# Kernel optimization log

Hardware: AMD Instinct MI355X
Metric: run time of the kernel (lower is better)

The kernel has to match this reference:

```python
import jax, jax.numpy as jnp
import numpy as np

NEG_SLOPE = 0.01  # torch nn.LeakyReLU default


def setup_inputs() -> dict:
    key = jax.random.key(0)
    k1, k2, k3, k4, k5 = jax.random.split(key, 5)
    B, C, N, O = 32, 512, 1024, 512
    x = jax.random.normal(k1, (B, C, N), dtype=jnp.float32)
    wq = jax.random.normal(k2, (C,), dtype=jnp.float32) * (1.0 / np.sqrt(C))
    wk = jax.random.normal(k3, (C,), dtype=jnp.float32) * (1.0 / np.sqrt(C))
    wm = jax.random.normal(k4, (O, C), dtype=jnp.float32) * (1.0 / np.sqrt(C))
    bm = jax.random.normal(k5, (O,), dtype=jnp.float32) * 0.01
    return {"x": x, "wq": wq, "wk": wk, "wm": wm, "bm": bm}


def reference(x, wq, wk, wm, bm):
    # x: [B, C, N]
    q = jnp.einsum('c,bcn->bn', wq, x)            # [B, N] (Conv1d C->1, k=1, no bias)
    k = jnp.einsum('c,bcn->bn', wk, x)            # [B, N]
    scores = q[:, None, :] + k[:, :, None]        # [B, N, N] additive broadcast
    scores = jnp.where(scores > 0, scores, NEG_SLOPE * scores)  # LeakyReLU
    att = jax.nn.softmax(scores, axis=-1)         # softmax over last dim
    agg = jnp.einsum('bcn,bmn->bcm', x, att)      # weighted aggregation [B, C, N]
    out = jnp.einsum('oc,bcm->bom', wm, agg) + bm[None, :, None]  # Conv1d k=1
    return jax.nn.relu(out)
```

## Files before the change

### kernel.cpp

```cpp
#include <hip/hip_runtime.h>


constexpr int B = 32, C = 512, N = 1024, O = 512;
constexpr float L2E = 1.4426950408889634f;

typedef _Float16 half8 __attribute__((ext_vector_type(8)));
typedef _Float16 half4v __attribute__((ext_vector_type(4)));
typedef _Float16 half2v __attribute__((ext_vector_type(2)));
typedef float f32x4 __attribute__((ext_vector_type(4)));
typedef float f32x16 __attribute__((ext_vector_type(16)));

#if __has_builtin(__builtin_amdgcn_exp2f)
#define EXP2(x) __builtin_amdgcn_exp2f(x)
#else
#define EXP2(x) exp2f(x)
#endif

__device__ __forceinline__ half8 cvt8(float4 a, float4 b) {
  half8 h;
  h[0] = (_Float16)a.x; h[1] = (_Float16)a.y; h[2] = (_Float16)a.z; h[3] = (_Float16)a.w;
  h[4] = (_Float16)b.x; h[5] = (_Float16)b.y; h[6] = (_Float16)b.z; h[7] = (_Float16)b.w;
  return h;
}

__device__ __forceinline__ unsigned fenc(float x) {
  unsigned u = __float_as_uint(x);
  return (u & 0x80000000u) ? ~u : (u ^ 0x80000000u);
}
__device__ __forceinline__ float fdec(unsigned e) {
  unsigned u = (e & 0x80000000u) ? (e ^ 0x80000000u) : ~e;
  return __uint_as_float(u);
}

__global__ __launch_bounds__(256) void wmh_kernel(const float* __restrict__ wm,
                                                  _Float16* __restrict__ wmh,
                                                  unsigned* __restrict__ qmax_u) {
  int i = (blockIdx.x * 256 + threadIdx.x) * 8;
  float4 a = *(const float4*)(wm + i);
  float4 b = *(const float4*)(wm + i + 4);
  *(half8*)(wmh + i) = cvt8(a, b);
  if (blockIdx.x == 0 && threadIdx.x < 64) qmax_u[threadIdx.x] = 0u;
}

__global__ __launch_bounds__(256) void gemm_y_kernel(const float* __restrict__ x,
    const _Float16* __restrict__ wmh, const float* __restrict__ wq,
    const float* __restrict__ wk, float* __restrict__ q, float* __restrict__ k,
    unsigned* __restrict__ qmax_u, _Float16* __restrict__ Yt) {
  __shared__ half2v Xs[2][16 * 130];
  __shared__ float mred[4];
  int b  = blockIdx.y;
  int n0 = blockIdx.x * 128;
  int o0 = blockIdx.z * 128;
  int t = threadIdx.x;
  int w = t >> 6, l = t & 63;
  int nw = w >> 1, ow = w & 1;
  int lm = l & 15, q8 = (l >> 4) * 8, q4 = (l >> 4) * 4;

  int cp = t >> 4, ng = t & 15;
  bool doqk = (blockIdx.z == 0);
  float aq[8] = {}, ak[8] = {};

  const _Float16* wb[4];
#pragma unroll
  for (int j = 0; j < 4; ++j)
    wb[j] = wmh + (size_t)(o0 + ow * 64 + j * 16 + lm) * C + q8;
  const float* xbase = x + ((size_t)b * C + 2 * cp) * N + n0 + ng * 8;

  float4 a0 = *(const float4*)(xbase);
  float4 a1 = *(const float4*)(xbase + 4);
  float4 b0 = *(const float4*)(xbase + N);
  float4 b1 = *(const float4*)(xbase + N + 4);
  half8 bf[4];
#pragma unroll
  for (int j = 0; j < 4; ++j) bf[j] = *(const half8*)(wb[j]);

  if (doqk) {
    float2 wq2 = *(const float2*)&wq[2 * cp];
    float2 wk2 = *(const float2*)&wk[2 * cp];
    aq[0] = fmaf(wq2.x, a0.x, fmaf(wq2.y, b0.x, aq[0]));
    aq[1] = fmaf(wq2.x, a0.y, fmaf(wq2.y, b0.y, aq[1]));
    aq[2] = fmaf(wq2.x, a0.z, fmaf(wq2.y, b0.z, aq[2]));
    aq[3] = fmaf(wq2.x, a0.w, fmaf(wq2.y, b0.w, aq[3]));
    aq[4] = fmaf(wq2.x, a1.x, fmaf(wq2.y, b1.x, aq[4]));
    aq[5] = fmaf(wq2.x, a1.y, fmaf(wq2.y, b1.y, aq[5]));
    aq[6] = fmaf(wq2.x, a1.z, fmaf(wq2.y, b1.z, aq[6]));
    aq[7] = fmaf(wq2.x, a1.w, fmaf(wq2.y, b1.w, aq[7]));
    ak[0] = fmaf(wk2.x, a0.x, fmaf(wk2.y, b0.x, ak[0]));
    ak[1] = fmaf(wk2.x, a0.y, fmaf(wk2.y, b0.y, ak[1]));
    ak[2] = fmaf(wk2.x, a0.z, fmaf(wk2.y, b0.z, ak[2]));
    ak[3] = fmaf(wk2.x, a0.w, fmaf(wk2.y, b0.w, ak[3]));
    ak[4] = fmaf(wk2.x, a1.x, fmaf(wk2.y, b1.x, ak[4]));
    ak[5] = fmaf(wk2.x, a1.y, fmaf(wk2.y, b1.y, ak[5]));
    ak[6] = fmaf(wk2.x, a1.z, fmaf(wk2.y, b1.z, ak[6]));
    ak[7] = fmaf(wk2.x, a1.w, fmaf(wk2.y, b1.w, ak[7]));
  }
  {
    half2v* xp = &Xs[0][cp * 130 + ng * 8];
    xp[0] = half2v{(_Float16)a0.x, (_Float16)b0.x};
    xp[1] = half2v{(_Float16)a0.y, (_Float16)b0.y};
    xp[2] = half2v{(_Float16)a0.z, (_Float16)b0.z};
    xp[3] = half2v{(_Float16)a0.w, (_Float16)b0.w};
    xp[4] = half2v{(_Float16)a1.x, (_Float16)b1.x};
    xp[5] = half2v{(_Float16)a1.y, (_Float16)b1.y};
    xp[6] = half2v{(_Float16)a1.z, (_Float16)b1.z};
    xp[7] = half2v{(_Float16)a1.w, (_Float16)b1.w};
  }
  __syncthreads();

  f32x4 acc[4][4] = {};
  for (int it = 0; it < 16; ++it) {
    int p = it & 1;
    float4 na0, na1, nb0, nb1;
    half8 nbf[4];
    if (it < 15) {
      int c1 = (it + 1) * 32;
      const float* xr = xbase + (size_t)c1 * N;
      na0 = *(const float4*)(xr);
      na1 = *(const float4*)(xr + 4);
      nb0 = *(const float4*)(xr + N);
      nb1 = *(const float4*)(xr + N + 4);
#pragma unroll
      for (int j = 0; j < 4; ++j) nbf[j] = *(const half8*)(wb[j] + c1);
    }
    half8 af[4];
#pragma unroll
    for (int i = 0; i < 4; ++i) {
      int nrow = nw * 64 + i * 16 + lm;
#pragma unroll
      for (int jp = 0; jp < 4; ++jp) {
        half2v pr = Xs[p][(q4 + jp) * 130 + nrow];
        af[i][2 * jp]     = pr[0];
        af[i][2 * jp + 1] = pr[1];
      }
    }
#pragma unroll
    for (int i = 0; i < 4; ++i)
#pragma unroll
      for (int j = 0; j < 4; ++j)
        acc[i][j] = __builtin_amdgcn_mfma_f32_16x16x32_f16(af[i], bf[j], acc[i][j], 0, 0, 0);

    if (it < 15) {
      int c1 = (it + 1) * 32;
      if (doqk) {
        float2 wq2 = *(const float2*)&wq[c1 + 2 * cp];
        float2 wk2 = *(const float2*)&wk[c1 + 2 * cp];
        aq[0] = fmaf(wq2.x, na0.x, fmaf(wq2.y, nb0.x, aq[0]));
        aq[1] = fmaf(wq2.x, na0.y, fmaf(wq2.y, nb0.y, aq[1]));
        aq[2] = fmaf(wq2.x, na0.z, fmaf(wq2.y, nb0.z, aq[2]));
        aq[3] = fmaf(wq2.x, na0.w, fmaf(wq2.y, nb0.w, aq[3]));
        aq[4] = fmaf(wq2.x, na1.x, fmaf(wq2.y, nb1.x, aq[4]));
        aq[5] = fmaf(wq2.x, na1.y, fmaf(wq2.y, nb1.y, aq[5]));
        aq[6] = fmaf(wq2.x, na1.z, fmaf(wq2.y, nb1.z, aq[6]));
        aq[7] = fmaf(wq2.x, na1.w, fmaf(wq2.y, nb1.w, aq[7]));
        ak[0] = fmaf(wk2.x, na0.x, fmaf(wk2.y, nb0.x, ak[0]));
        ak[1] = fmaf(wk2.x, na0.y, fmaf(wk2.y, nb0.y, ak[1]));
        ak[2] = fmaf(wk2.x, na0.z, fmaf(wk2.y, nb0.z, ak[2]));
        ak[3] = fmaf(wk2.x, na0.w, fmaf(wk2.y, nb0.w, ak[3]));
        ak[4] = fmaf(wk2.x, na1.x, fmaf(wk2.y, nb1.x, ak[4]));
        ak[5] = fmaf(wk2.x, na1.y, fmaf(wk2.y, nb1.y, ak[5]));
        ak[6] = fmaf(wk2.x, na1.z, fmaf(wk2.y, nb1.z, ak[6]));
        ak[7] = fmaf(wk2.x, na1.w, fmaf(wk2.y, nb1.w, ak[7]));
      }
      half2v* xp = &Xs[p ^ 1][cp * 130 + ng * 8];
      xp[0] = half2v{(_Float16)na0.x, (_Float16)nb0.x};
      xp[1] = half2v{(_Float16)na0.y, (_Float16)nb0.y};
      xp[2] = half2v{(_Float16)na0.z, (_Float16)nb0.z};
      xp[3] = half2v{(_Float16)na0.w, (_Float16)nb0.w};
      xp[4] = half2v{(_Float16)na1.x, (_Float16)nb1.x};
      xp[5] = half2v{(_Float16)na1.y, (_Float16)nb1.y};
      xp[6] = half2v{(_Float16)na1.z, (_Float16)nb1.z};
      xp[7] = half2v{(_Float16)na1.w, (_Float16)nb1.w};
#pragma unroll
      for (int j = 0; j < 4; ++j) bf[j] = nbf[j];
    }
    __syncthreads();
  }

#pragma unroll
  for (int i = 0; i < 4; ++i) {
    int n_b = n0 + nw * 64 + i * 16 + (l >> 4) * 4;
#pragma unroll
    for (int j = 0; j < 4; ++j) {
      int o_c = o0 + ow * 64 + j * 16 + lm;
      half4v h;
      h[0] = (_Float16)acc[i][j][0];
      h[1] = (_Float16)acc[i][j][1];
      h[2] = (_Float16)acc[i][j][2];
      h[3] = (_Float16)acc[i][j][3];
      *(half4v*)&Yt[((size_t)b * O + o_c) * N + n_b] = h;
    }
  }

  if (doqk) {
    float* red = (float*)Xs;
    float qv_final = -1e30f;
    __syncthreads();
#pragma unroll
    for (int j = 0; j < 8; ++j) red[cp * 130 + ng * 8 + j] = aq[j];
    __syncthreads();
    if (t < 128) {
      float s = 0.f;
#pragma unroll
      for (int p = 0; p < 16; ++p) s += red[p * 130 + t];
      qv_final = L2E * s;
      q[b * N + n0 + t] = qv_final;
    }
    __syncthreads();
#pragma unroll
    for (int j = 0; j < 8; ++j) red[cp * 130 + ng * 8 + j] = ak[j];
    __syncthreads();
    if (t < 128) {
      float s = 0.f;
#pragma unroll
      for (int p = 0; p < 16; ++p) s += red[p * 130 + t];
      k[b * N + n0 + t] = L2E * s;
    }
    float m = qv_final;
#pragma unroll
    for (int off = 32; off > 0; off >>= 1) m = fmaxf(m, __shfl_down(m, off, 64));
    if ((t & 63) == 0) mred[t >> 6] = m;
    __syncthreads();
    if (t == 0) {
      float bmax = fmaxf(fmaxf(mred[0], mred[1]), fmaxf(mred[2], mred[3]));
      atomicMax(&qmax_u[b], fenc(bmax));
    }
  }
}

__global__ __launch_bounds__(512) void gemm_out_kernel(const _Float16* __restrict__ Yt,
    const float* __restrict__ q, const float* __restrict__ k,
    const unsigned* __restrict__ qmax_u, const float* __restrict__ bm,
    float* __restrict__ out) {
  __shared__ __align__(16) float qs[N];
  __shared__ __align__(16) _Float16 Ys[2][256 * 40];
  __shared__ float izs[256];
  int b  = blockIdx.y;
  int o0 = blockIdx.x * 256;
  int m0 = blockIdx.z * 256;
  int t = threadIdx.x;
  int w = t >> 6, l = t & 63;
  int ml = l & 31, g2 = l >> 5;

  *(float2*)&qs[t * 2] = *(const float2*)&q[b * N + t * 2];

  float qmv = fdec(qmax_u[b]);
  float km = k[b * N + m0 + w * 32 + ml];
  float s0 = qmv + km;
  float M  = fmaxf(s0, 0.01f * s0);
  float kc2 = km - M;
  float kc3 = fmaf(0.01f, km, -M);

  half8 ones;
#pragma unroll
  for (int jj = 0; jj < 8; ++jj) ones[jj] = (_Float16)1.0f;
  f32x16 acc_z = {};
  int yr = t >> 1, yp = t & 1;
  const _Float16* ysrc = Yt + ((size_t)b * O + o0 + yr) * N + yp * 16;

  {
    half8 z0 = *(const half8*)(ysrc);
    half8 z1 = *(const half8*)(ysrc + 8);
    *(half8*)&Ys[0][yr * 40 + yp * 16]     = z0;
    *(half8*)&Ys[0][yr * 40 + yp * 16 + 8] = z1;
  }
  __syncthreads();

  f32x16 acc[8] = {};
  for (int it = 0; it < N / 32; ++it) {
    int p = it & 1;
    int n0k = it * 32;
    half8 z0, z1;
    if (it < N / 32 - 1) {
      z0 = *(const half8*)(ysrc + n0k + 32);
      z1 = *(const half8*)(ysrc + n0k + 40);
    }
#pragma unroll
    for (int kh = 0; kh < 2; ++kh) {
      float4 qa = *(const float4*)&qs[n0k + kh * 16 + g2 * 8];
      float4 qb = *(const float4*)&qs[n0k + kh * 16 + g2 * 8 + 4];
      float qv[8] = {qa.x, qa.y, qa.z, qa.w, qb.x, qb.y, qb.z, qb.w};
      half8 af;
#pragma unroll
      for (int jj = 0; jj < 8; ++jj) {
        float arg = fmaxf(qv[jj] + kc2, fmaf(0.01f, qv[jj], kc3));
        af[jj] = (_Float16)EXP2(arg);
      }
      acc_z = __builtin_amdgcn_mfma_f32_32x32x16_f16(af, ones, acc_z, 0, 0, 0);
#pragma unroll
      for (int s = 0; s < 8; ++s) {
        half8 bf = *(const half8*)&Ys[p][(s * 32 + ml) * 40 + kh * 16 + g2 * 8];
        acc[s] = __builtin_amdgcn_mfma_f32_32x32x16_f16(af, bf, acc[s], 0, 0, 0);
      }
    }
    if (it < N / 32 - 1) {
      *(half8*)&Ys[p ^ 1][yr * 40 + yp * 16]     = z0;
      *(half8*)&Ys[p ^ 1][yr * 40 + yp * 16 + 8] = z1;
    }
    __syncthreads();
  }

  if (ml == 0) {
#pragma unroll
    for (int rq = 0; rq < 4; ++rq)
#pragma unroll
      for (int r = 0; r < 4; ++r)
        izs[w * 32 + r + 8 * rq + 4 * g2] = 1.0f / acc_z[rq * 4 + r];
  }
  __syncthreads();

  float4 izv[4];
#pragma unroll
  for (int rq = 0; rq < 4; ++rq)
    izv[rq] = *(const float4*)&izs[w * 32 + 8 * rq + 4 * g2];

#pragma unroll
  for (int s = 0; s < 8; ++s) {
    int o_c = o0 + s * 32 + ml;
    float bias = bm[o_c];
#pragma unroll
    for (int rq = 0; rq < 4; ++rq) {
      int m_b = m0 + w * 32 + 8 * rq + 4 * g2;
      float4 r;
      r.x = fmaxf(fmaf(acc[s][rq * 4 + 0], izv[rq].x, bias), 0.f);
      r.y = fmaxf(fmaf(acc[s][rq * 4 + 1], izv[rq].y, bias), 0.f);
      r.z = fmaxf(fmaf(acc[s][rq * 4 + 2], izv[rq].z, bias), 0.f);
      r.w = fmaxf(fmaf(acc[s][rq * 4 + 3], izv[rq].w, bias), 0.f);
      *(float4*)&out[((size_t)b * O + o_c) * N + m_b] = r;
    }
  }
}

extern "C" void kernel_launch(void* const* d_in, const int* in_sizes, int n_in,
                              void* d_out, int out_size, void* d_ws, size_t ws_size,
                              hipStream_t stream) {
  const float* x  = (const float*)d_in[0];
  const float* wq = (const float*)d_in[1];
  const float* wk = (const float*)d_in[2];
  const float* wm = (const float*)d_in[3];
  const float* bm = (const float*)d_in[4];
  float* out = (float*)d_out;

  float* q    = (float*)d_ws;
  float* k    = q + B * N;
  unsigned* qmax_u = (unsigned*)(k + B * N);
  _Float16* wmh = (_Float16*)(qmax_u + 64);
  _Float16* Yt  = wmh + (size_t)O * C;

  wmh_kernel<<<dim3(O * C / (256 * 8)), 256, 0, stream>>>(wm, wmh, qmax_u);
  gemm_y_kernel<<<dim3(N / 128, B, O / 128), 256, 0, stream>>>(x, wmh, wq, wk, q, k, qmax_u, Yt);
  gemm_out_kernel<<<dim3(O / 256, B, N / 256), 512, 0, stream>>>(Yt, q, k, qmax_u, bm, out);
}
```

Measured before the change: 205.7 us.

## Split x fp16 transpose into prep kernel and load GEMM tiles via global_load_lds

A new prep kernel converts x to fp16 once, transposed to [B,N,C], and computes q, k and the per-batch q max there, so that work leaves the GEMM. The Y GEMM then streams A tiles directly into LDS with global_load_lds and uses contiguous half8 LDS reads instead of per-element half2 gathers. It also remaps block indices so that tiles sharing data land on the same XCD. The cost is an extra kernel launch and a full fp16 copy of x written to and read back from global memory, using the output buffer as scratch. The original GEMM re-read and re-converted x for each of its four O tiles.

Result: slower. 214.8 us (+4.4%).

```diff
diff --git a/kernel.cpp b/kernel.cpp
--- a/kernel.cpp
+++ b/kernel.cpp
@@ -30,6 +30,12 @@
 __device__ __forceinline__ float fdec(unsigned e) {
   unsigned u = (e & 0x80000000u) ? (e ^ 0x80000000u) : ~e;
   return __uint_as_float(u);
+}
+
+__device__ __forceinline__ void gload16(const _Float16* g, _Float16* l) {
+  __builtin_amdgcn_global_load_lds(
+      (const __attribute__((address_space(1))) unsigned int*)(g),
+      (__attribute__((address_space(3))) unsigned int*)(l), 16, 0, 0);
 }
 
 __global__ __launch_bounds__(256) void wmh_kernel(const float* __restrict__ wm,
@@ -42,41 +48,31 @@
   if (blockIdx.x == 0 && threadIdx.x < 64) qmax_u[threadIdx.x] = 0u;
 }
 
-__global__ __launch_bounds__(256) void gemm_y_kernel(const float* __restrict__ x,
-    const _Float16* __restrict__ wmh, const float* __restrict__ wq,
-    const float* __restrict__ wk, float* __restrict__ q, float* __restrict__ k,
-    unsigned* __restrict__ qmax_u, _Float16* __restrict__ Yt) {
-  __shared__ half2v Xs[2][16 * 130];
-  __shared__ float mred[4];
+__global__ __launch_bounds__(256) void prep_kernel(const float* __restrict__ x,
+    const float* __restrict__ wq, const float* __restrict__ wk,
+    float* __restrict__ q, float* __restrict__ k, unsigned* __restrict__ qmax_u,
+    _Float16* __restrict__ xhT) {
+  __shared__ half2v Ts[32 * 67];
   int b  = blockIdx.y;
-  int n0 = blockIdx.x * 128;
-  int o0 = blockIdx.z * 128;
+  int n0 = blockIdx.x * 64;
   int t = threadIdx.x;
-  int w = t >> 6, l = t & 63;
-  int nw = w >> 1, ow = w & 1;
-  int lm = l & 15, q8 = (l >> 4) * 8, q4 = (l >> 4) * 4;
-
-  int cp = t >> 4, ng = t & 15;
-  bool doqk = (blockIdx.z == 0);
+  int cp = t >> 3;
+  int ng = t & 7;
+  const float* xbase = x + ((size_t)b * C + 2 * cp) * N + n0 + ng * 8;
+  int nl = t >> 2;
+  int hq = t & 3;
+  _Float16* xout = xhT + ((size_t)b * N + n0 + nl) * C + hq * 16;
   float aq[8] = {}, ak[8] = {};
 
-  const _Float16* wb[4];
-#pragma unroll
-  for (int j = 0; j < 4; ++j)
-    wb[j] = wmh + (size_t)(o0 + ow * 64 + j * 16 + lm) * C + q8;
-  const float* xbase = x + ((size_t)b * C + 2 * cp) * N + n0 + ng * 8;
-
-  float4 a0 = *(const float4*)(xbase);
-  float4 a1 = *(const float4*)(xbase + 4);
-  float4 b0 = *(const float4*)(xbase + N);
-  float4 b1 = *(const float4*)(xbase + N + 4);
-  half8 bf[4];
-#pragma unroll
-  for (int j = 0; j < 4; ++j) bf[j] = *(const half8*)(wb[j]);
-
-  if (doqk) {
-    float2 wq2 = *(const float2*)&wq[2 * cp];
-    float2 wk2 = *(const float2*)&wk[2 * cp];
+  for (int ch = 0; ch < 8; ++ch) {
+    int c0 = ch * 64;
+    const float* xr = xbase + (size_t)c0 * N;
+    float4 a0 = *(const float4*)(xr);
+    float4 a1 = *(const float4*)(xr + 4);
+    float4 b0 = *(const float4*)(xr + N);
+    float4 b1 = *(const float4*)(xr + N + 4);
+    float2 wq2 = *(const float2*)&wq[c0 + 2 * cp];
+    float2 wk2 = *(const float2*)&wk[c0 + 2 * cp];
     aq[0] = fmaf(wq2.x, a0.x, fmaf(wq2.y, b0.x, aq[0]));
     aq[1] = fmaf(wq2.x, a0.y, fmaf(wq2.y, b0.y, aq[1]));
     aq[2] = fmaf(wq2.x, a0.z, fmaf(wq2.y, b0.z, aq[2]));
@@ -93,92 +89,118 @@
     ak[5] = fmaf(wk2.x, a1.y, fmaf(wk2.y, b1.y, ak[5]));
     ak[6] = fmaf(wk2.x, a1.z, fmaf(wk2.y, b1.z, ak[6]));
     ak[7] = fmaf(wk2.x, a1.w, fmaf(wk2.y, b1.w, ak[7]));
-  }
-  {
-    half2v* xp = &Xs[0][cp * 130 + ng * 8];
-    xp[0] = half2v{(_Float16)a0.x, (_Float16)b0.x};
-    xp[1] = half2v{(_Float16)a0.y, (_Float16)b0.y};
-    xp[2] = half2v{(_Float16)a0.z, (_Float16)b0.z};
-    xp[3] = half2v{(_Float16)a0.w, (_Float16)b0.w};
-    xp[4] = half2v{(_Float16)a1.x, (_Float16)b1.x};
-    xp[5] = half2v{(_Float16)a1.y, (_Float16)b1.y};
-    xp[6] = half2v{(_Float16)a1.z, (_Float16)b1.z};
-    xp[7] = half2v{(_Float16)a1.w, (_Float16)b1.w};
-  }
+    {
+      half2v* xp = &Ts[cp * 67 + ng * 8];
+      xp[0] = half2v{(_Float16)a0.x, (_Float16)b0.x};
+      xp[1] = half2v{(_Float16)a0.y, (_Float16)b0.y};
+      xp[2] = half2v{(_Float16)a0.z, (_Float16)b0.z};
+      xp[3] = half2v{(_Float16)a0.w, (_Float16)b0.w};
+      xp[4] = half2v{(_Float16)a1.x, (_Float16)b1.x};
+      xp[5] = half2v{(_Float16)a1.y, (_Float16)b1.y};
+      xp[6] = half2v{(_Float16)a1.z, (_Float16)b1.z};
+      xp[7] = half2v{(_Float16)a1.w, (_Float16)b1.w};
+    }
+    __syncthreads();
+    half8 o0h, o1h;
+#pragma unroll
+    for (int u = 0; u < 4; ++u) {
+      half2v pr = Ts[(hq * 8 + u) * 67 + nl];
+      o0h[2 * u] = pr[0]; o0h[2 * u + 1] = pr[1];
+    }
+#pragma unroll
+    for (int u = 4; u < 8; ++u) {
+      half2v pr = Ts[(hq * 8 + u) * 67 + nl];
+      o1h[2 * (u - 4)] = pr[0]; o1h[2 * (u - 4) + 1] = pr[1];
+    }
+    *(half8*)(xout + c0)     = o0h;
+    *(half8*)(xout + c0 + 8) = o1h;
+    __syncthreads();
+  }
+
+  float* red = (float*)Ts;
+#pragma unroll
+  for (int j = 0; j < 8; ++j) red[cp * 67 + ng * 8 + j] = aq[j];
+  __syncthreads();
+  float qv = -1e30f;
+  if (t < 64) {
+    float s = 0.f;
+#pragma unroll
+    for (int p = 0; p < 32; ++p) s += red[p * 67 + t];
+    qv = L2E * s;
+    q[b * N + n0 + t] = qv;
+  }
+  __syncthreads();
+#pragma unroll
+  for (int j = 0; j < 8; ++j) red[cp * 67 + ng * 8 + j] = ak[j];
+  __syncthreads();
+  if (t < 64) {
+    float s = 0.f;
+#pragma unroll
+    for (int p = 0; p < 32; ++p) s += red[p * 67 + t];
+    k[b * N + n0 + t] = L2E * s;
+    float m = qv;
+#pragma unroll
+    for (int off = 32; off > 0; off >>= 1) m = fmaxf(m, __shfl_down(m, off, 64));
+    if (t == 0) atomicMax(&qmax_u[b], fenc(m));
+  }
+}
+
+__global__ __launch_bounds__(256) void gemm_y_kernel(const _Float16* __restrict__ xhT,
+    const _Float16* __restrict__ wmh, _Float16* __restrict__ Yt) {
+  __shared__ __align__(16) _Float16 As[2][128 * 32];
+  int f = blockIdx.x;
+  int xcd = f & 7, g = f >> 3;
+  int o_id = g & 3;
+  int p2 = xcd * 32 + (g >> 2);
+  int n_id = p2 & 7, b = p2 >> 3;
+  int n0 = n_id * 128, o0 = o_id * 128;
+  int t = threadIdx.x;
+  int w = t >> 6, l = t & 63;
+  int nw = w >> 1, ow = w & 1;
+  int lm = l & 15, q8 = (l >> 4) * 8, q4 = (l >> 4) * 4;
+
+  const _Float16* asrc[2];
+#pragma unroll
+  for (int m = 0; m < 2; ++m) {
+    int u = m * 256 + t;
+    asrc[m] = xhT + ((size_t)b * N + n0 + (u >> 2)) * C + (u & 3) * 8;
+  }
+  const _Float16* wb[4];
+#pragma unroll
+  for (int j = 0; j < 4; ++j)
+    wb[j] = wmh + (size_t)(o0 + ow * 64 + j * 16 + lm) * C + q8;
+
+#pragma unroll
+  for (int m = 0; m < 2; ++m)
+    gload16(asrc[m], &As[0][(m * 256 + (t & ~63)) * 8]);
   __syncthreads();
 
   f32x4 acc[4][4] = {};
   for (int it = 0; it < 16; ++it) {
     int p = it & 1;
-    float4 na0, na1, nb0, nb1;
-    half8 nbf[4];
     if (it < 15) {
       int c1 = (it + 1) * 32;
-      const float* xr = xbase + (size_t)c1 * N;
-      na0 = *(const float4*)(xr);
-      na1 = *(const float4*)(xr + 4);
-      nb0 = *(const float4*)(xr + N);
-      nb1 = *(const float4*)(xr + N + 4);
-#pragma unroll
-      for (int j = 0; j < 4; ++j) nbf[j] = *(const half8*)(wb[j] + c1);
-    }
-    half8 af[4];
+#pragma unroll
+      for (int m = 0; m < 2; ++m)
+        gload16(asrc[m] + c1, &As[p ^ 1][(m * 256 + (t & ~63)) * 8]);
+    }
+    int c0 = it * 32;
+    half8 bf[4];
+#pragma unroll
+    for (int j = 0; j < 4; ++j) bf[j] = *(const half8*)(wb[j] + c0);
 #pragma unroll
     for (int i = 0; i < 4; ++i) {
-      int nrow = nw * 64 + i * 16 + lm;
-#pragma unroll
-      for (int jp = 0; jp < 4; ++jp) {
-        half2v pr = Xs[p][(q4 + jp) * 130 + nrow];
-        af[i][2 * jp]     = pr[0];
-        af[i][2 * jp + 1] = pr[1];
-      }
-    }
-#pragma unroll
-    for (int i = 0; i < 4; ++i)
+      half8 af = *(const half8*)&As[p][(nw * 64 + i * 16 + lm) * 32 + q8];
 #pragma unroll
       for (int j = 0; j < 4; ++j)
-        acc[i][j] = __builtin_amdgcn_mfma_f32_16x16x32_f16(af[i], bf[j], acc[i][j], 0, 0, 0);
-
-    if (it < 15) {
-      int c1 = (it + 1) * 32;
-      if (doqk) {
-        float2 wq2 = *(const float2*)&wq[c1 + 2 * cp];
-        float2 wk2 = *(const float2*)&wk[c1 + 2 * cp];
-        aq[0] = fmaf(wq2.x, na0.x, fmaf(wq2.y, nb0.x, aq[0]));
-        aq[1] = fmaf(wq2.x, na0.y, fmaf(wq2.y, nb0.y, aq[1]));
-        aq[2] = fmaf(wq2.x, na0.z, fmaf(wq2.y, nb0.z, aq[2]));
-        aq[3] = fmaf(wq2.x, na0.w, fmaf(wq2.y, nb0.w, aq[3]));
-        aq[4] = fmaf(wq2.x, na1.x, fmaf(wq2.y, nb1.x, aq[4]));
-        aq[5] = fmaf(wq2.x, na1.y, fmaf(wq2.y, nb1.y, aq[5]));
-        aq[6] = fmaf(wq2.x, na1.z, fmaf(wq2.y, nb1.z, aq[6]));
-        aq[7] = fmaf(wq2.x, na1.w, fmaf(wq2.y, nb1.w, aq[7]));
-        ak[0] = fmaf(wk2.x, na0.x, fmaf(wk2.y, nb0.x, ak[0]));
-        ak[1] = fmaf(wk2.x, na0.y, fmaf(wk2.y, nb0.y, ak[1]));
-        ak[2] = fmaf(wk2.x, na0.z, fmaf(wk2.y, nb0.z, ak[2]));
-        ak[3] = fmaf(wk2.x, na0.w, fmaf(wk2.y, nb0.w, ak[3]));
-        ak[4] = fmaf(wk2.x, na1.x, fmaf(wk2.y, nb1.x, ak[4]));
-        ak[5] = fmaf(wk2.x, na1.y, fmaf(wk2.y, nb1.y, ak[5]));
-        ak[6] = fmaf(wk2.x, na1.z, fmaf(wk2.y, nb1.z, ak[6]));
-        ak[7] = fmaf(wk2.x, na1.w, fmaf(wk2.y, nb1.w, ak[7]));
-      }
-      half2v* xp = &Xs[p ^ 1][cp * 130 + ng * 8];
-      xp[0] = half2v{(_Float16)na0.x, (_Float16)nb0.x};
-      xp[1] = half2v{(_Float16)na0.y, (_Float16)nb0.y};
-      xp[2] = half2v{(_Float16)na0.z, (_Float16)nb0.z};
-      xp[3] = half2v{(_Float16)na0.w, (_Float16)nb0.w};
-      xp[4] = half2v{(_Float16)na1.x, (_Float16)nb1.x};
-      xp[5] = half2v{(_Float16)na1.y, (_Float16)nb1.y};
-      xp[6] = half2v{(_Float16)na1.z, (_Float16)nb1.z};
-      xp[7] = half2v{(_Float16)na1.w, (_Float16)nb1.w};
-#pragma unroll
-      for (int j = 0; j < 4; ++j) bf[j] = nbf[j];
+        acc[i][j] = __builtin_amdgcn_mfma_f32_16x16x32_f16(af, bf[j], acc[i][j], 0, 0, 0);
     }
     __syncthreads();
   }
 
 #pragma unroll
   for (int i = 0; i < 4; ++i) {
-    int n_b = n0 + nw * 64 + i * 16 + (l >> 4) * 4;
+    int n_b = n0 + nw * 64 + i * 16 + q4;
 #pragma unroll
     for (int j = 0; j < 4; ++j) {
       int o_c = o0 + ow * 64 + j * 16 + lm;
@@ -188,41 +210,6 @@
       h[2] = (_Float16)acc[i][j][2];
       h[3] = (_Float16)acc[i][j][3];
       *(half4v*)&Yt[((size_t)b * O + o_c) * N + n_b] = h;
-    }
-  }
-
-  if (doqk) {
-    float* red = (float*)Xs;
-    float qv_final = -1e30f;
-    __syncthreads();
-#pragma unroll
-    for (int j = 0; j < 8; ++j) red[cp * 130 + ng * 8 + j] = aq[j];
-    __syncthreads();
-    if (t < 128) {
-      float s = 0.f;
-#pragma unroll
-      for (int p = 0; p < 16; ++p) s += red[p * 130 + t];
-      qv_final = L2E * s;
-      q[b * N + n0 + t] = qv_final;
-    }
-    __syncthreads();
-#pragma unroll
-    for (int j = 0; j < 8; ++j) red[cp * 130 + ng * 8 + j] = ak[j];
-    __syncthreads();
-    if (t < 128) {
-      float s = 0.f;
-#pragma unroll
-      for (int p = 0; p < 16; ++p) s += red[p * 130 + t];
-      k[b * N + n0 + t] = L2E * s;
-    }
-    float m = qv_final;
-#pragma unroll
-    for (int off = 32; off > 0; off >>= 1) m = fmaxf(m, __shfl_down(m, off, 64));
-    if ((t & 63) == 0) mred[t >> 6] = m;
-    __syncthreads();
-    if (t == 0) {
-      float bmax = fmaxf(fmaxf(mred[0], mred[1]), fmaxf(mred[2], mred[3]));
-      atomicMax(&qmax_u[b], fenc(bmax));
     }
   }
 }
@@ -345,8 +332,10 @@
   unsigned* qmax_u = (unsigned*)(k + B * N);
   _Float16* wmh = (_Float16*)(qmax_u + 64);
   _Float16* Yt  = wmh + (size_t)O * C;
+  _Float16* xhT = (_Float16*)d_out;
 
   wmh_kernel<<<dim3(O * C / (256 * 8)), 256, 0, stream>>>(wm, wmh, qmax_u);
-  gemm_y_kernel<<<dim3(N / 128, B, O / 128), 256, 0, stream>>>(x, wmh, wq, wk, q, k, qmax_u, Yt);
+  prep_kernel<<<dim3(N / 64, B), 256, 0, stream>>>(x, wq, wk, q, k, qmax_u, xhT);
+  gemm_y_kernel<<<dim3(1024), 256, 0, stream>>>(xhT, wmh, Yt);
   gemm_out_kernel<<<dim3(O / 256, B, N / 256), 512, 0, stream>>>(Yt, q, k, qmax_u, bm, out);
 }
```
